# Kernel optimization log

Measured on AMD Instinct MI355X. Metric: run time of the kernel, lower is better.

The kernel has to match this reference:

```python
import jax, jax.numpy as jnp
import numpy as np


def setup_inputs() -> dict:
    key = jax.random.key(0)
    k1, k2, k3 = jax.random.split(key, 3)
    B, S, D = 8, 2048, 1024
    lstm_output = jax.random.normal(k1, (B, S, D), dtype=jnp.float32)
    W = jax.random.normal(k2, (D, D), dtype=jnp.float32) * (1.0 / np.sqrt(D))
    b = jax.random.normal(k3, (D,), dtype=jnp.float32) * 0.01
    return {"lstm_output": lstm_output, "W": W, "b": b}


def reference(lstm_output, W, b):
    # proj(x) = x @ W^T + b  (torch nn.Linear convention: W is [out, in])
    proj = jnp.einsum('bsd,ed->bse', lstm_output, W) + b          # [B,S,D]
    # scores[b,i,j] = x[b,i] . proj[b,j]
    attn_scores = jnp.einsum('bid,bjd->bij', lstm_output, proj)   # [B,S,S]
    attn_weights = jax.nn.softmax(attn_scores, axis=-1)           # [B,S,S]
    context_vector = jnp.einsum('bij,bjd->bid', attn_weights, lstm_output)
    return (context_vector, attn_weights)
```

## Files before the change

### kernel.cpp

```cpp
#include <hip/hip_runtime.h>


typedef _Float16 f16;
typedef _Float16 f16x8 __attribute__((ext_vector_type(8)));
typedef _Float16 f16x4 __attribute__((ext_vector_type(4)));
typedef float f32x4 __attribute__((ext_vector_type(4)));
typedef unsigned int u32;

#define AS1 __attribute__((address_space(1)))
#define AS3 __attribute__((address_space(3)))

static constexpr int Bb = 8, Ss = 2048, Dd = 1024;

__global__ __launch_bounds__(256) void split_cast_k(
    const float* __restrict__ in, f16* __restrict__ hi, f16* __restrict__ lo,
    size_t n4) {
  size_t i = (size_t)blockIdx.x * 256 + threadIdx.x;
  if (i >= n4) return;
  float4 v = ((const float4*)in)[i];
  f16x4 h, l;
  h[0] = (f16)v.x; l[0] = (f16)(v.x - (float)h[0]);
  h[1] = (f16)v.y; l[1] = (f16)(v.y - (float)h[1]);
  h[2] = (f16)v.z; l[2] = (f16)(v.z - (float)h[2]);
  h[3] = (f16)v.w; l[3] = (f16)(v.w - (float)h[3]);
  ((f16x4*)hi)[i] = h;
  ((f16x4*)lo)[i] = l;
}

__global__ __launch_bounds__(256) void cast_k(const float* __restrict__ in,
                                              f16* __restrict__ out,
                                              size_t n4) {
  size_t i = (size_t)blockIdx.x * 256 + threadIdx.x;
  if (i >= n4) return;
  float4 v = ((const float4*)in)[i];
  f16x4 h;
  h[0] = (f16)v.x; h[1] = (f16)v.y; h[2] = (f16)v.z; h[3] = (f16)v.w;
  ((f16x4*)out)[i] = h;
}

__global__ __launch_bounds__(256) void transpose_cast_k(
    const float* __restrict__ x, f16* __restrict__ xT) {
  __shared__ f16 tile[32][33];
  const int b = blockIdx.z;
  const int s0 = blockIdx.x * 32, d0 = blockIdx.y * 32;
  const int tx = threadIdx.x & 31, ty = threadIdx.x >> 5;
  const float* xb = x + (size_t)b * Ss * Dd;
#pragma unroll
  for (int r = 0; r < 32; r += 8)
    tile[ty + r][tx] = (f16)xb[(size_t)(s0 + ty + r) * Dd + d0 + tx];
  __syncthreads();
  f16* xTb = xT + (size_t)b * Dd * Ss;
#pragma unroll
  for (int r = 0; r < 32; r += 8)
    xTb[(size_t)(d0 + ty + r) * Ss + s0 + tx] = tile[tx][ty + r];
}

template <int PPW>
__device__ __forceinline__ void stage_tile(const f16* __restrict__ g,
                                           size_t ld, f16* lds, int wave,
                                           int lane) {
#pragma unroll
  for (int c = 0; c < PPW; ++c) {
    int panel = wave * PPW + c;
    const f16* gp =
        g + (size_t)(panel * 16 + (lane & 15)) * ld + (lane >> 4) * 8;
    AS3 u32* lp = (AS3 u32*)(lds + panel * 512);
    __builtin_amdgcn_global_load_lds((const AS1 u32*)gp, lp, 16, 0, 0);
  }
}

template <bool DUAL_A, bool OUT_F16>
__global__ __launch_bounds__(512, 2) void gemm_bt(
    const f16* __restrict__ A0, const f16* __restrict__ A1,
    const f16* __restrict__ B0, float* __restrict__ C, f16* __restrict__ Ch,
    const float* __restrict__ bias, int K, size_t ldc, size_t sA, size_t sB,
    size_t sC) {
  extern __shared__ f16 smem[];
  const int tid = threadIdx.x;
  const int wave = tid >> 6, lane = tid & 63;
  const size_t tn = (size_t)blockIdx.x * 256;
  const size_t tm = (size_t)blockIdx.y * 256;
  const int b = blockIdx.z;

  constexpr int STAGE = (DUAL_A ? 3 : 2) * 8192;
  constexpr int BOFF = DUAL_A ? 16384 : 8192;

  const f16* Ah = A0 + (size_t)b * sA + tm * (size_t)K;
  const f16* Al = DUAL_A ? (A1 + (size_t)b * sA + tm * (size_t)K) : nullptr;
  const f16* Bp = B0 + (size_t)b * sB + tn * (size_t)K;

  const int wr = wave >> 1, wc = wave & 1;
  const int pA = wr * 4;
  const int pB = wc * 8;

  f16* b0 = smem;
  f16* b1 = smem + STAGE;
  f16* b2 = smem + 2 * STAGE;

  auto stage_all = [&](int k, f16* buf) {
    stage_tile<2>(Ah + k, K, buf, wave, lane);
    if constexpr (DUAL_A) stage_tile<2>(Al + k, K, buf + 8192, wave, lane);
    stage_tile<2>(Bp + k, K, buf + BOFF, wave, lane);
  };

  f32x4 acc[4][8] = {};

  const int nIter = K / 32;
  stage_all(0, b0);
  stage_all(32, b1);
  for (int it = 0; it < nIter; ++it) {
    if (it < nIter - 1) {
      if constexpr (DUAL_A)
        asm volatile("s_waitcnt vmcnt(6)" ::: "memory");
      else
        asm volatile("s_waitcnt vmcnt(4)" ::: "memory");
    } else {
      asm volatile("s_waitcnt vmcnt(0)" ::: "memory");
    }
    __builtin_amdgcn_s_barrier();
    asm volatile("" ::: "memory");
    if (it + 2 < nIter) stage_all((it + 2) * 32, b2);

    f16x8 ah[4], al[4];
#pragma unroll
    for (int i = 0; i < 4; ++i) {
      ah[i] = *(const f16x8*)&b0[(pA + i) * 512 + lane * 8];
      if constexpr (DUAL_A)
        al[i] = *(const f16x8*)&b0[8192 + (pA + i) * 512 + lane * 8];
    }
    __builtin_amdgcn_s_setprio(1);
#pragma unroll
    for (int j = 0; j < 8; ++j) {
      f16x8 bf = *(const f16x8*)&b0[BOFF + (pB + j) * 512 + lane * 8];
#pragma unroll
      for (int i = 0; i < 4; ++i) {
        acc[i][j] =
            __builtin_amdgcn_mfma_f32_16x16x32_f16(ah[i], bf, acc[i][j], 0, 0, 0);
        if constexpr (DUAL_A)
          acc[i][j] = __builtin_amdgcn_mfma_f32_16x16x32_f16(al[i], bf,
                                                             acc[i][j], 0, 0, 0);
      }
    }
    __builtin_amdgcn_s_setprio(0);
    f16* t = b0; b0 = b1; b1 = b2; b2 = t;
  }

  const int wm = wr * 64, wn = wc * 128;
#pragma unroll
  for (int i = 0; i < 4; ++i) {
    size_t row0 = tm + wm + i * 16 + ((lane >> 4) << 2);
#pragma unroll
    for (int j = 0; j < 8; ++j) {
      size_t col = tn + wn + j * 16 + (lane & 15);
      float bj = bias ? bias[col] : 0.f;
#pragma unroll
      for (int r = 0; r < 4; ++r) {
        float v = acc[i][j][r] + bj;
        size_t off = (size_t)b * sC + (row0 + r) * ldc + col;
        if constexpr (OUT_F16)
          Ch[off] = (f16)v;
        else
          C[off] = v;
      }
    }
  }
}

__global__ __launch_bounds__(256) void softmax_k(float* __restrict__ sc,
                                                 f16* __restrict__ wh) {
  const size_t row = blockIdx.x;
  float* p = sc + row * 2048;
  f16* w = wh + row * 2048;
  const int t = threadIdx.x;
  float4 v0 = ((const float4*)p)[t];
  float4 v1 = ((const float4*)p)[256 + t];
  float m = fmaxf(fmaxf(fmaxf(v0.x, v0.y), fmaxf(v0.z, v0.w)),
                  fmaxf(fmaxf(v1.x, v1.y), fmaxf(v1.z, v1.w)));
#pragma unroll
  for (int o = 32; o; o >>= 1) m = fmaxf(m, __shfl_xor(m, o, 64));
  __shared__ float red[4];
  if ((t & 63) == 0) red[t >> 6] = m;
  __syncthreads();
  m = fmaxf(fmaxf(red[0], red[1]), fmaxf(red[2], red[3]));
  v0.x = __expf(v0.x - m);
  v0.y = __expf(v0.y - m);
  v0.z = __expf(v0.z - m);
  v0.w = __expf(v0.w - m);
  v1.x = __expf(v1.x - m);
  v1.y = __expf(v1.y - m);
  v1.z = __expf(v1.z - m);
  v1.w = __expf(v1.w - m);
  float s = v0.x + v0.y + v0.z + v0.w + v1.x + v1.y + v1.z + v1.w;
#pragma unroll
  for (int o = 32; o; o >>= 1) s += __shfl_xor(s, o, 64);
  __shared__ float red2[4];
  if ((t & 63) == 0) red2[t >> 6] = s;
  __syncthreads();
  s = red2[0] + red2[1] + red2[2] + red2[3];
  float inv = 1.0f / s;
  v0.x *= inv; v0.y *= inv; v0.z *= inv; v0.w *= inv;
  v1.x *= inv; v1.y *= inv; v1.z *= inv; v1.w *= inv;
  ((float4*)p)[t] = v0;
  ((float4*)p)[256 + t] = v1;
  f16x4 h0, h1;
  h0[0] = (f16)v0.x; h0[1] = (f16)v0.y; h0[2] = (f16)v0.z; h0[3] = (f16)v0.w;
  h1[0] = (f16)v1.x; h1[1] = (f16)v1.y; h1[2] = (f16)v1.z; h1[3] = (f16)v1.w;
  ((f16x4*)w)[t] = h0;
  ((f16x4*)w)[256 + t] = h1;
}

extern "C" void kernel_launch(void* const* d_in, const int* in_sizes, int n_in,
                              void* d_out, int out_size, void* d_ws,
                              size_t ws_size, hipStream_t stream) {
  (void)in_sizes; (void)n_in; (void)out_size; (void)ws_size;
  const float* x = (const float*)d_in[0];
  const float* W = (const float*)d_in[1];
  const float* bias = (const float*)d_in[2];
  float* ctx = (float*)d_out;
  float* scores = (float*)d_out + (size_t)Bb * Ss * Dd;

  const size_t nBSD = (size_t)Bb * Ss * Dd;
  const size_t nDD = (size_t)Dd * Dd;

  f16* p = (f16*)d_ws;
  f16* x_hi = p; p += nBSD;
  f16* x_lo = p; p += nBSD;
  f16* xT   = p; p += nBSD;
  f16* W_hi = p; p += nDD;
  f16* p_hi = p; p += nBSD;
  f16* attnw = x_hi;

  static bool attr_done = false;
  if (!attr_done) {
    hipFuncSetAttribute(reinterpret_cast<const void*>(&gemm_bt<true, true>),
                        hipFuncAttributeMaxDynamicSharedMemorySize, 147456);
    hipFuncSetAttribute(reinterpret_cast<const void*>(&gemm_bt<true, false>),
                        hipFuncAttributeMaxDynamicSharedMemorySize, 147456);
    hipFuncSetAttribute(reinterpret_cast<const void*>(&gemm_bt<false, false>),
                        hipFuncAttributeMaxDynamicSharedMemorySize, 147456);
    attr_done = true;
  }
  constexpr unsigned LDS_DUAL = 3u * 24576u * 2u;
  constexpr unsigned LDS_SINGLE = 3u * 16384u * 2u;

  split_cast_k<<<(unsigned)(nBSD / 4 / 256), 256, 0, stream>>>(x, x_hi, x_lo,
                                                               nBSD / 4);
  cast_k<<<(unsigned)(nDD / 4 / 256), 256, 0, stream>>>(W, W_hi, nDD / 4);
  transpose_cast_k<<<dim3(Ss / 32, Dd / 32, Bb), 256, 0, stream>>>(x, xT);

  gemm_bt<true, true>
      <<<dim3(Dd / 256, (Bb * Ss) / 256, 1), 512, LDS_DUAL, stream>>>(
          x_hi, x_lo, W_hi, nullptr, p_hi, bias, Dd, (size_t)Dd, 0, 0, 0);

  gemm_bt<true, false>
      <<<dim3(Ss / 256, Ss / 256, Bb), 512, LDS_DUAL, stream>>>(
          x_hi, x_lo, p_hi, scores, nullptr, nullptr, Dd, (size_t)Ss,
          (size_t)Ss * Dd, (size_t)Ss * Dd, (size_t)Ss * Ss);

  softmax_k<<<Bb * Ss, 256, 0, stream>>>(scores, attnw);

  gemm_bt<false, false>
      <<<dim3(Dd / 256, Ss / 256, Bb), 512, LDS_SINGLE, stream>>>(
          attnw, nullptr, xT, ctx, nullptr, nullptr, Ss, (size_t)Dd,
          (size_t)Ss * Ss, (size_t)Dd * Ss, (size_t)Ss * Dd);
}
```

Baseline: 577.1 us.

## Split GEMM main loop into two barrier-separated phases interleaving loads and MFMA

```diff
diff --git a/kernel.cpp b/kernel.cpp
--- a/kernel.cpp
+++ b/kernel.cpp
@@ -9,6 +9,14 @@
 
 #define AS1 __attribute__((address_space(1)))
 #define AS3 __attribute__((address_space(3)))
+
+#define FENCE() asm volatile("" ::: "memory")
+#define BARRIER()                  \
+  do {                             \
+    FENCE();                       \
+    __builtin_amdgcn_s_barrier();  \
+    FENCE();                       \
+  } while (0)
 
 static constexpr int Bb = 8, Ss = 2048, Dd = 1024;
 
@@ -97,17 +105,19 @@
   f16* b1 = smem + STAGE;
   f16* b2 = smem + 2 * STAGE;
 
-  auto stage_all = [&](int k, f16* buf) {
+  auto stageA = [&](int k, f16* buf) {
     stage_tile<2>(Ah + k, K, buf, wave, lane);
     if constexpr (DUAL_A) stage_tile<2>(Al + k, K, buf + 8192, wave, lane);
+  };
+  auto stageB = [&](int k, f16* buf) {
     stage_tile<2>(Bp + k, K, buf + BOFF, wave, lane);
   };
 
   f32x4 acc[4][8] = {};
 
   const int nIter = K / 32;
-  stage_all(0, b0);
-  stage_all(32, b1);
+  stageA(0, b0); stageB(0, b0);
+  stageA(32, b1); stageB(32, b1);
   for (int it = 0; it < nIter; ++it) {
     if (it < nIter - 1) {
       if constexpr (DUAL_A)
@@ -117,31 +127,63 @@
     } else {
       asm volatile("s_waitcnt vmcnt(0)" ::: "memory");
     }
-    __builtin_amdgcn_s_barrier();
-    asm volatile("" ::: "memory");
-    if (it + 2 < nIter) stage_all((it + 2) * 32, b2);
-
-    f16x8 ah[4], al[4];
-#pragma unroll
-    for (int i = 0; i < 4; ++i) {
+    BARRIER();
+
+    f16x8 ah[4], al[4], bf[4];
+#pragma unroll
+    for (int i = 0; i < 4; ++i)
       ah[i] = *(const f16x8*)&b0[(pA + i) * 512 + lane * 8];
-      if constexpr (DUAL_A)
+#pragma unroll
+    for (int j = 0; j < 4; ++j)
+      bf[j] = *(const f16x8*)&b0[BOFF + (pB + j) * 512 + lane * 8];
+    if constexpr (DUAL_A) {
+#pragma unroll
+      for (int i = 0; i < 4; ++i)
         al[i] = *(const f16x8*)&b0[8192 + (pA + i) * 512 + lane * 8];
     }
+    if (it + 2 < nIter) stageA((it + 2) * 32, b2);
+    BARRIER();
     __builtin_amdgcn_s_setprio(1);
 #pragma unroll
-    for (int j = 0; j < 8; ++j) {
-      f16x8 bf = *(const f16x8*)&b0[BOFF + (pB + j) * 512 + lane * 8];
-#pragma unroll
-      for (int i = 0; i < 4; ++i) {
+    for (int j = 0; j < 4; ++j)
+#pragma unroll
+      for (int i = 0; i < 4; ++i)
         acc[i][j] =
-            __builtin_amdgcn_mfma_f32_16x16x32_f16(ah[i], bf, acc[i][j], 0, 0, 0);
-        if constexpr (DUAL_A)
-          acc[i][j] = __builtin_amdgcn_mfma_f32_16x16x32_f16(al[i], bf,
+            __builtin_amdgcn_mfma_f32_16x16x32_f16(ah[i], bf[j], acc[i][j], 0, 0, 0);
+    if constexpr (DUAL_A) {
+#pragma unroll
+      for (int j = 0; j < 4; ++j)
+#pragma unroll
+        for (int i = 0; i < 4; ++i)
+          acc[i][j] = __builtin_amdgcn_mfma_f32_16x16x32_f16(al[i], bf[j],
                                                              acc[i][j], 0, 0, 0);
-      }
     }
     __builtin_amdgcn_s_setprio(0);
+
+    BARRIER();
+    f16x8 bg[4];
+#pragma unroll
+    for (int j = 0; j < 4; ++j)
+      bg[j] = *(const f16x8*)&b0[BOFF + (pB + 4 + j) * 512 + lane * 8];
+    if (it + 2 < nIter) stageB((it + 2) * 32, b2);
+    BARRIER();
+    __builtin_amdgcn_s_setprio(1);
+#pragma unroll
+    for (int j = 0; j < 4; ++j)
+#pragma unroll
+      for (int i = 0; i < 4; ++i)
+        acc[i][4 + j] = __builtin_amdgcn_mfma_f32_16x16x32_f16(
+            ah[i], bg[j], acc[i][4 + j], 0, 0, 0);
+    if constexpr (DUAL_A) {
+#pragma unroll
+      for (int j = 0; j < 4; ++j)
+#pragma unroll
+        for (int i = 0; i < 4; ++i)
+          acc[i][4 + j] = __builtin_amdgcn_mfma_f32_16x16x32_f16(
+              al[i], bg[j], acc[i][4 + j], 0, 0, 0);
+    }
+    __builtin_amdgcn_s_setprio(0);
+
     f16* t = b0; b0 = b1; b1 = b2; b2 = t;
   }
 
```

After: 570.9 us. No clear change (-1.1%).
